# Kernel optimization log

Measured on AMD Instinct MI355X. Metric: run time of the kernel, lower is better.

Reference implementation:

```python
import jax, jax.numpy as jnp
import numpy as np

N_HEADS = 16
MAX_DIST = 64


def setup_inputs() -> dict:
    key = jax.random.key(0)
    ks = jax.random.split(key, 7)
    B, S, D = 16, 512, 1024
    hd = D // N_HEADS
    num_rel = 2 * MAX_DIST + 1
    s = 0.02
    return {
        "x": jax.random.normal(ks[0], (B, S, D), dtype=jnp.float32),
        "Wq": jax.random.normal(ks[1], (D, D), dtype=jnp.float32) * s,
        "Wk": jax.random.normal(ks[2], (D, D), dtype=jnp.float32) * s,
        "Wv": jax.random.normal(ks[3], (D, D), dtype=jnp.float32) * s,
        "Eq": jax.random.normal(ks[4], (num_rel, hd), dtype=jnp.float32) * s,
        "Ek": jax.random.normal(ks[5], (num_rel, hd), dtype=jnp.float32) * s,
        "Ev": jax.random.normal(ks[6], (num_rel, hd), dtype=jnp.float32) * s,
    }


def reference(x, Wq, Wk, Wv, Eq, Ek, Ev):
    B, S, D = x.shape
    H = N_HEADS
    hd = D // H
    # relative position index matrix, values in [0, 2*max_dist]
    r = jnp.arange(S)
    rel = jnp.clip(r[:, None] - r[None, :], -MAX_DIST, MAX_DIST) + MAX_DIST  # (S,S)

    def proj(W):
        return jnp.einsum('bsd,de->bse', x, W).reshape(B, S, H, hd).transpose(0, 2, 1, 3)

    q, k, v = proj(Wq), proj(Wk), proj(Wv)  # (B,H,S,hd)

    a_q = Eq[rel]  # (S,S,hd)
    a_k = Ek[rel]
    a_v = Ev[rel]

    content = jnp.einsum('bhld,bhmd->bhlm', q, k)
    rel_k = jnp.einsum('bhld,lmd->bhlm', q, a_k)
    rel_q = jnp.einsum('bhmd,lmd->bhlm', k, a_q)
    pos_pos = jnp.einsum('lmd,lmd->lm', a_q, a_k)

    scale = 1.0 / (hd ** 0.5)
    logits = (content + rel_k + rel_q + pos_pos) * scale
    attn = jax.nn.softmax(logits, axis=-1)

    out = jnp.einsum('bhlm,bhmd->bhld', attn, v) + jnp.einsum('bhlm,lmd->bhld', attn, a_v)
    return out.transpose(0, 2, 1, 3).reshape(B, S, D)
```

## Files before the change

kernel.cpp:

```cpp
#include <hip/hip_runtime.h>

#define SEQ 512
#define NH 16
#define HD 64
#define NREL 129
#define ER 136
#define SCALE 0.125f

typedef __attribute__((ext_vector_type(8))) short bf16x8;
typedef __attribute__((ext_vector_type(4))) float f32x4;

__device__ __forceinline__ unsigned short f2bf(float x) {
    unsigned u = __builtin_bit_cast(unsigned, x);
    u += 0x7FFFu + ((u >> 16) & 1u);
    return (unsigned short)(u >> 16);
}
__device__ __forceinline__ float bf2f(unsigned short s) {
    unsigned u = ((unsigned)s) << 16;
    return __builtin_bit_cast(float, u);
}
__device__ __forceinline__ unsigned pack2(float a, float b) {
    return (unsigned)f2bf(a) | ((unsigned)f2bf(b) << 16);
}
__device__ __forceinline__ void gld_lds16(const uint4* g, uint4* l) {
    __builtin_amdgcn_global_load_lds(
        (const __attribute__((address_space(1))) unsigned int*)(g),
        (__attribute__((address_space(3))) unsigned int*)(l),
        16, 0, 0);
}

__global__ __launch_bounds__(256) void conv_x(const float* __restrict__ in,
                                              unsigned short* __restrict__ ob) {
    size_t i = (size_t)blockIdx.x * 256 + threadIdx.x;
    const float4* p = (const float4*)in + i * 2;
    float4 a = p[0], b = p[1];
    uint4 o;
    o.x = pack2(a.x, a.y); o.y = pack2(a.z, a.w);
    o.z = pack2(b.x, b.y); o.w = pack2(b.z, b.w);
    ((uint4*)ob)[i] = o;
}

__global__ __launch_bounds__(256) void conv_w(const float* __restrict__ Wq,
                                              const float* __restrict__ Wk,
                                              const float* __restrict__ Wv,
                                              unsigned short* __restrict__ WbT) {
    __shared__ float Ws[64][65];
    const int t = threadIdx.x;
    const int mi = blockIdx.x >> 8;
    const int rem = blockIdx.x & 255;
    const int k0 = (rem >> 4) * 64, n0 = (rem & 15) * 64;
    const float* W = mi == 0 ? Wq : (mi == 1 ? Wk : Wv);
    const int rr = t >> 4, c4 = (t & 15) * 4;
#pragma unroll
    for (int j = 0; j < 4; j++) {
        float4 v = *(const float4*)&W[(size_t)(k0 + rr + j * 16) * 1024 + n0 + c4];
        Ws[rr + j * 16][c4 + 0] = v.x; Ws[rr + j * 16][c4 + 1] = v.y;
        Ws[rr + j * 16][c4 + 2] = v.z; Ws[rr + j * 16][c4 + 3] = v.w;
    }
    __syncthreads();
    const int n = t >> 2;
    for (int cc = (t & 3); cc < 8; cc += 4) {
        unsigned short tmp[8];
#pragma unroll
        for (int j = 0; j < 8; j++) tmp[j] = f2bf(Ws[cc * 8 + j][n]);
        *(uint4*)&WbT[(size_t)(mi * 1024 + n0 + n) * 1024 + k0 + cc * 8] = *(uint4*)tmp;
    }
}

__global__ void conv_e(const float* __restrict__ Eq, const float* __restrict__ Ek,
                       unsigned short* __restrict__ Eqb, unsigned short* __restrict__ Ekb) {
    const int t = threadIdx.x;
    for (int i = t; i < 1152; i += 256) {
        int r = i >> 3, c8 = (i & 7) * 8;
        uint4 oq = {0, 0, 0, 0}, ok = {0, 0, 0, 0};
        if (r < NREL) {
            float4 a = *(const float4*)&Eq[r * 64 + c8];
            float4 b = *(const float4*)&Eq[r * 64 + c8 + 4];
            oq.x = pack2(a.x, a.y); oq.y = pack2(a.z, a.w);
            oq.z = pack2(b.x, b.y); oq.w = pack2(b.z, b.w);
            float4 c = *(const float4*)&Ek[r * 64 + c8];
            float4 d = *(const float4*)&Ek[r * 64 + c8 + 4];
            ok.x = pack2(c.x, c.y); ok.y = pack2(c.z, c.w);
            ok.z = pack2(d.x, d.y); ok.w = pack2(d.z, d.w);
        }
        ((uint4*)Eqb)[i] = oq;
        ((uint4*)Ekb)[i] = ok;
    }
}

__global__ void ee_k(const float* __restrict__ Eq, const float* __restrict__ Ek,
                     float* __restrict__ ee) {
    int r = threadIdx.x;
    if (r < NREL) {
        float s = 0.f;
        for (int d = 0; d < HD; d++) s += Eq[r * HD + d] * Ek[r * HD + d];
        ee[r] = s;
    }
}

__global__ __launch_bounds__(256) void proj_mfma(const unsigned short* __restrict__ xb,
                                                 const unsigned short* __restrict__ WbT,
                                                 unsigned short* __restrict__ Qb,
                                                 unsigned short* __restrict__ Kb,
                                                 unsigned short* __restrict__ Vb) {
    __shared__ uint4 smem[2176];
    const int t = threadIdx.x;
    const int bm = blockIdx.x & 63;
    const int bn = blockIdx.x >> 6;
    const int m0 = bm * 128;
    const int n0g = bn * 128;
    const int w = t >> 6, lane = t & 63, ln = lane & 15, kg = lane >> 4;
    const int wm = w >> 1, wn = w & 1;
    const int lrow = lane >> 3;
    const int lcol = lane & 7;

    f32x4 acc[4][4];
#pragma unroll
    for (int i = 0; i < 4; i++)
#pragma unroll
        for (int j = 0; j < 4; j++) acc[i][j] = (f32x4){0.f, 0.f, 0.f, 0.f};

    const uint4* gA[4]; const uint4* gB[4]; uint4* lA[4]; uint4* lB[4];
#pragma unroll
    for (int j = 0; j < 4; j++) {
        const int seg = w * 4 + j;
        gA[j] = (const uint4*)xb  + (size_t)(m0  + seg * 8 + lrow) * 128 + lcol;
        gB[j] = (const uint4*)WbT + (size_t)(n0g + seg * 8 + lrow) * 128 + lcol;
        lA[j] = smem + seg * 64;
        lB[j] = smem + 1024 + seg * 64;
    }

    for (int kt = 0; kt < 16; ++kt) {
        __syncthreads();
#pragma unroll
        for (int j = 0; j < 4; j++) {
            gld_lds16(gA[j] + kt * 8, lA[j]);
            gld_lds16(gB[j] + kt * 8, lB[j]);
        }
        __syncthreads();
#pragma unroll
        for (int ks = 0; ks < 2; ks++) {
            bf16x8 af[4], bfr[4];
            const int ch = ks * 4 + kg;
#pragma unroll
            for (int i = 0; i < 4; i++) af[i]  = *(const bf16x8*)(smem + (wm * 64 + i * 16 + ln) * 8 + ch);
#pragma unroll
            for (int j = 0; j < 4; j++) bfr[j] = *(const bf16x8*)(smem + 1024 + (wn * 64 + j * 16 + ln) * 8 + ch);
#pragma unroll
            for (int i = 0; i < 4; i++)
#pragma unroll
                for (int j = 0; j < 4; j++)
                    acc[i][j] = __builtin_amdgcn_mfma_f32_16x16x32_bf16(af[i], bfr[j], acc[i][j], 0, 0, 0);
        }
    }
    __syncthreads();
    short (*cs)[136] = (short(*)[136])smem;
#pragma unroll
    for (int i = 0; i < 4; i++)
#pragma unroll
        for (int j = 0; j < 4; j++)
#pragma unroll
            for (int reg = 0; reg < 4; reg++)
                cs[wm * 64 + i * 16 + kg * 4 + reg][wn * 64 + j * 16 + ln] = (short)f2bf(acc[i][j][reg]);
    __syncthreads();
    const int which = n0g >> 10;
    unsigned short* outp = which == 0 ? Qb : (which == 1 ? Kb : Vb);
    const int ncol0 = n0g & 1023;
#pragma unroll
    for (int j = 0; j < 8; j++) {
        int id = j * 256 + t;
        int r = id >> 4, c = id & 15;
        *((uint4*)(outp + (size_t)(m0 + r) * 1024 + ncol0) + c) = *((const uint4*)&cs[r][0] + c);
    }
}

__global__ __launch_bounds__(256) void qk_e_mfma(const unsigned short* __restrict__ Qb,
                                                 const unsigned short* __restrict__ Kb,
                                                 const unsigned short* __restrict__ Ekb,
                                                 const unsigned short* __restrict__ Eqb,
                                                 const float* __restrict__ ee,
                                                 unsigned short* __restrict__ qEe,
                                                 unsigned short* __restrict__ kEb) {
    __shared__ uint4 lds[3328];
    __shared__ float eeS[136];
    uint4* Qt = lds;
    uint4* Kt = lds + 512;
    uint4* EkS = lds + 1024;
    uint4* EqS = lds + 2176;
    const int t = threadIdx.x, w = t >> 6, lane = t & 63, ln = lane & 15, kg = lane >> 4;
    const int g0 = blockIdx.x * 64;

    {
        int r = t >> 2, cb = (t & 3) * 2;
        const uint4* qg = (const uint4*)Qb + (size_t)(g0 + r) * 8;
        const uint4* kgp = (const uint4*)Kb + (size_t)(g0 + r) * 8;
#pragma unroll
        for (int j = 0; j < 2; j++) {
            int c = cb + j;
            Qt[r * 8 + (c ^ (r & 7))] = qg[c];
            Kt[r * 8 + (c ^ (r & 7))] = kgp[c];
        }
    }
    for (int i = t; i < 1152; i += 256) {
        int r = i >> 3, c = i & 7;
        EkS[r * 8 + (c ^ (r & 7))] = ((const uint4*)Ekb)[i];
        EqS[r * 8 + (c ^ (r & 7))] = ((const uint4*)Eqb)[i];
    }
    if (t < NREL) eeS[t] = ee[t];
    __syncthreads();

    const int lx = ln & 7;
    {
        bf16x8 a0 = *(bf16x8*)&Qt[(w * 16 + ln) * 8 + (kg ^ lx)];
        bf16x8 a1 = *(bf16x8*)&Qt[(w * 16 + ln) * 8 + ((4 + kg) ^ lx)];
        f32x4 acc[9];
#pragma unroll
        for (int j = 0; j < 9; j++) acc[j] = (f32x4){0.f, 0.f, 0.f, 0.f};
#pragma unroll
        for (int j = 0; j < 9; j++) {
            acc[j] = __builtin_amdgcn_mfma_f32_16x16x32_bf16(a0, *(bf16x8*)&EkS[(j * 16 + ln) * 8 + (kg ^ lx)], acc[j], 0, 0, 0);
            acc[j] = __builtin_amdgcn_mfma_f32_16x16x32_bf16(a1, *(bf16x8*)&EkS[(j * 16 + ln) * 8 + ((4 + kg) ^ lx)], acc[j], 0, 0, 0);
        }
#pragma unroll
        for (int j = 0; j < 9; j++) {
            int r = j * 16 + ln;
            if (r <= 128) {
#pragma unroll
                for (int reg = 0; reg < 4; reg++) {
                    int g = g0 + w * 16 + kg * 4 + reg;
                    qEe[(size_t)g * ER + r] = f2bf(acc[j][reg] + eeS[r]);
                }
            }
        }
    }
    {
        bf16x8 a0 = *(bf16x8*)&Kt[(w * 16 + ln) * 8 + (kg ^ lx)];
        bf16x8 a1 = *(bf16x8*)&Kt[(w * 16 + ln) * 8 + ((4 + kg) ^ lx)];
        f32x4 acc[9];
#pragma unroll
        for (int j = 0; j < 9; j++) acc[j] = (f32x4){0.f, 0.f, 0.f, 0.f};
#pragma unroll
        for (int j = 0; j < 9; j++) {
            acc[j] = __builtin_amdgcn_mfma_f32_16x16x32_bf16(a0, *(bf16x8*)&EqS[(j * 16 + ln) * 8 + (kg ^ lx)], acc[j], 0, 0, 0);
            acc[j] = __builtin_amdgcn_mfma_f32_16x16x32_bf16(a1, *(bf16x8*)&EqS[(j * 16 + ln) * 8 + ((4 + kg) ^ lx)], acc[j], 0, 0, 0);
        }
#pragma unroll
        for (int j = 0; j < 9; j++) {
            int r = j * 16 + ln;
            if (r <= 128) {
#pragma unroll
                for (int reg = 0; reg < 4; reg++) {
                    int g = g0 + w * 16 + kg * 4 + reg;
                    kEb[(size_t)g * ER + r] = f2bf(acc[j][reg]);
                }
            }
        }
    }
}

__global__ __launch_bounds__(256) void attn_k(const unsigned short* __restrict__ Q,
                                              const unsigned short* __restrict__ K,
                                              const unsigned short* __restrict__ V,
                                              const unsigned short* __restrict__ qEg,
                                              const unsigned short* __restrict__ kEg,
                                              const float* __restrict__ Ev,
                                              float* __restrict__ out) {
    __shared__ __align__(16) char un[18432];
    __shared__ short qEeS[64][ER];
    __shared__ short Pt[4][16][40];
    __shared__ short aRs[4][16][ER];
    __shared__ float invs[4][16];

    short (*Qsb)[64] = (short(*)[64])un;
    short (*Kt)[72]  = (short(*)[72])un;
    short* Vtt       = (short*)(un + 4608);
    short (*kEt)[ER] = (short(*)[ER])(un + 9728);
    short (*EvT)[ER] = (short(*)[ER])un;

    const int t = threadIdx.x;
    const int g = blockIdx.x;
    const int lt = (g >> 3) & 7;
    const int bh = ((g >> 6) << 3) | (g & 7);
    const int b = bh >> 4, h = bh & 15;
    const int bS = b * SEQ;
    const int l0 = lt * 64;
    const int w = t >> 6;
    const int lane = t & 63;
    const int ln = lane & 15;
    const int kg = lane >> 4;
    const int l0w = l0 + w * 16;

    for (int i = t; i < 512; i += 256) {
        int r = i >> 3, c8 = (i & 7) * 8;
        *(uint4*)&Qsb[r][c8] = *(const uint4*)&Q[(size_t)(bS + l0 + r) * 1024 + h * 64 + c8];
    }
    for (int i = t; i < 1088; i += 256) {
        int r = i / 17, c = i % 17;
        ((uint4*)&qEeS[r][0])[c] = ((const uint4*)&qEg[(size_t)((bS + l0 + r) * NH + h) * ER])[c];
    }
    for (int i = t; i < 4352; i += 256) ((unsigned*)aRs)[i] = 0u;
    __syncthreads();

    bf16x8 qf0 = *(bf16x8*)&Qsb[w * 16 + ln][kg * 8];
    bf16x8 qf1 = *(bf16x8*)&Qsb[w * 16 + ln][32 + kg * 8];

    const int sr = t >> 3;
    const int sc8 = (t & 7) * 8;
    const unsigned short* Kg0 = K + (size_t)(bS + sr) * 1024 + h * 64 + sc8;
    const unsigned short* Vg0 = V + (size_t)(bS + sr) * 1024 + h * 64 + sc8;
    const int r0 = t / 17,          c0 = t % 17;
    const int r1 = (t + 256) / 17,  c1 = (t + 256) % 17;
    const int r2 = (t + 512) / 17,  c2 = (t + 512) % 17;
    const unsigned short* kE0 = kEg + ((size_t)(bS + r0) * NH + h) * ER;
    const unsigned short* kE1 = kEg + ((size_t)(bS + r1) * NH + h) * ER;
    const unsigned short* kE2 = kEg + ((size_t)(bS + r2) * NH + h) * ER;

    uint4 kv, vv, ke0, ke1, ke2;
    kv  = *(const uint4*)(Kg0);
    vv  = *(const uint4*)(Vg0);
    ke0 = ((const uint4*)kE0)[c0];
    ke1 = ((const uint4*)kE1)[c1];
    if (t < 32) ke2 = ((const uint4*)kE2)[c2];

    f32x4 of[4];
#pragma unroll
    for (int nt = 0; nt < 4; nt++) of[nt] = (f32x4){0.f, 0.f, 0.f, 0.f};
    float rs[4]   = {0.f, 0.f, 0.f, 0.f};
    float s0[4]   = {0.f, 0.f, 0.f, 0.f};
    float s128[4] = {0.f, 0.f, 0.f, 0.f};

    const int vkey = (t & 7) & 3;
    for (int mt = 0; mt < 16; mt++) {
        const int m0 = mt * 32;
        __syncthreads();
        *(uint4*)&Kt[sr][sc8] = kv;
        {
            const short* vs = (const short*)&vv;
#pragma unroll
            for (int j = 0; j < 8; j++) {
                const int d = sc8 + j;
                Vtt[d * 40 + ((((sr >> 3) ^ vkey)) << 3) + (sr & 7)] = vs[j];
            }
        }
        ((uint4*)&kEt[r0][0])[c0] = ke0;
        ((uint4*)&kEt[r1][0])[c1] = ke1;
        if (t < 32) ((uint4*)&kEt[r2][0])[c2] = ke2;
        if (mt < 15) {
            const size_t koff = (size_t)(mt + 1) * 32 * 1024;
            const size_t eoff = (size_t)(mt + 1) * 32 * NH * ER;
            kv  = *(const uint4*)(Kg0 + koff);
            vv  = *(const uint4*)(Vg0 + koff);
            ke0 = ((const uint4*)(kE0 + eoff))[c0];
            ke1 = ((const uint4*)(kE1 + eoff))[c1];
            if (t < 32) ke2 = ((const uint4*)(kE2 + eoff))[c2];
        }
        __syncthreads();

#pragma unroll
        for (int sub = 0; sub < 2; sub++) {
            f32x4 acc = (f32x4){0.f, 0.f, 0.f, 0.f};
            acc = __builtin_amdgcn_mfma_f32_16x16x32_bf16(qf0, *(bf16x8*)&Kt[sub * 16 + ln][kg * 8], acc, 0, 0, 0);
            acc = __builtin_amdgcn_mfma_f32_16x16x32_bf16(qf1, *(bf16x8*)&Kt[sub * 16 + ln][32 + kg * 8], acc, 0, 0, 0);
            const int mloc = sub * 16 + ln;
            const int m = m0 + mloc;
#pragma unroll
            for (int reg = 0; reg < 4; reg++) {
                const int lr = kg * 4 + reg;
                const int dlt = (l0w + lr) - m;
                const int r = dlt < -64 ? 0 : (dlt > 64 ? 128 : dlt + 64);
                float lg = (acc[reg] + bf2f((unsigned short)qEeS[w * 16 + lr][r])
                                     + bf2f((unsigned short)kEt[mloc][r])) * SCALE;
                float p = __expf(lg);
                rs[reg] += p;
                if (dlt >= 64)       s128[reg] += p;
                else if (dlt <= -64) s0[reg]   += p;
                else                 aRs[w][lr][r] = (short)f2bf(p);
                Pt[w][lr][mloc] = (short)f2bf(p);
            }
        }
        asm volatile("" ::: "memory");
        bf16x8 pf = *(bf16x8*)&Pt[w][ln][kg * 8];
#pragma unroll
        for (int nt = 0; nt < 4; nt++) {
            const int d = nt * 16 + ln;
            const bf16x8 vf = *(const bf16x8*)&Vtt[d * 40 + ((kg ^ ((d >> 3) & 3)) << 3)];
            of[nt] = __builtin_amdgcn_mfma_f32_16x16x32_bf16(pf, vf, of[nt], 0, 0, 0);
        }
    }

    __syncthreads();
#pragma unroll
    for (int reg = 0; reg < 4; reg++) {
        for (int off = 1; off <= 8; off <<= 1) {
            rs[reg]   += __shfl_xor(rs[reg], off);
            s0[reg]   += __shfl_xor(s0[reg], off);
            s128[reg] += __shfl_xor(s128[reg], off);
        }
    }
    float inv[4];
#pragma unroll
    for (int reg = 0; reg < 4; reg++) inv[reg] = 1.0f / rs[reg];

    if (ln == 0) {
#pragma unroll
        for (int reg = 0; reg < 4; reg++) {
            aRs[w][kg * 4 + reg][0]   = (short)f2bf(s0[reg]   * inv[reg]);
            aRs[w][kg * 4 + reg][128] = (short)f2bf(s128[reg] * inv[reg]);
            invs[w][kg * 4 + reg] = inv[reg];
        }
    }
    for (int i = t; i < 8256; i += 256) {
        int r = i >> 6, d = i & 63;
        EvT[d][r] = (short)f2bf(Ev[i]);
    }
    __syncthreads();
    {
        const int row = lane >> 2;
        const float sc = invs[w][row];
#pragma unroll
        for (int kk = 0; kk < 32; kk++) {
            int c = (lane & 3) * 32 + kk;
            if (c >= 1) aRs[w][row][c] = (short)f2bf(bf2f((unsigned short)aRs[w][row][c]) * sc);
        }
    }
#pragma unroll
    for (int nt = 0; nt < 4; nt++)
#pragma unroll
        for (int reg = 0; reg < 4; reg++) of[nt][reg] *= inv[reg];
    __syncthreads();

    f32x4 o2[4];
#pragma unroll
    for (int nt = 0; nt < 4; nt++) o2[nt] = (f32x4){0.f, 0.f, 0.f, 0.f};
#pragma unroll
    for (int nt = 0; nt < 4; nt++)
#pragma unroll
        for (int ks = 0; ks < 4; ks++)
            o2[nt] = __builtin_amdgcn_mfma_f32_16x16x32_bf16(*(bf16x8*)&aRs[w][ln][ks * 32 + kg * 8],
                                                             *(bf16x8*)&EvT[nt * 16 + ln][ks * 32 + kg * 8],
                                                             o2[nt], 0, 0, 0);
#pragma unroll
    for (int nt = 0; nt < 4; nt++) {
        const float e128 = bf2f((unsigned short)EvT[nt * 16 + ln][128]);
#pragma unroll
        for (int reg = 0; reg < 4; reg++) {
            const int lr = kg * 4 + reg;
            const float a128 = bf2f((unsigned short)aRs[w][lr][128]);
            out[(size_t)(bS + l0w + lr) * 1024 + h * 64 + nt * 16 + ln] =
                of[nt][reg] + o2[nt][reg] + a128 * e128;
        }
    }
}

extern "C" void kernel_launch(void* const* d_in, const int* in_sizes, int n_in,
                              void* d_out, int out_size, void* d_ws, size_t ws_size,
                              hipStream_t stream) {
    const float* x  = (const float*)d_in[0];
    const float* Wq = (const float*)d_in[1];
    const float* Wk = (const float*)d_in[2];
    const float* Wv = (const float*)d_in[3];
    const float* Eq = (const float*)d_in[4];
    const float* Ek = (const float*)d_in[5];
    const float* Ev = (const float*)d_in[6];
    float* out = (float*)d_out;
    char* ws = (char*)d_ws;

    unsigned short* Qb  = (unsigned short*)(ws);
    unsigned short* Kb  = (unsigned short*)(ws + 16777216ull);
    unsigned short* Vb  = (unsigned short*)(ws + 33554432ull);
    unsigned short* xb  = (unsigned short*)(ws + 50331648ull);
    unsigned short* WbT = (unsigned short*)(ws + 67108864ull);
    unsigned short* Ekb = (unsigned short*)(ws + 73400320ull);
    unsigned short* Eqb = (unsigned short*)(ws + 73418752ull);
    float*          ee  = (float*)(ws + 73437184ull);
    unsigned short* qEe = (unsigned short*)(ws + 73437760ull);
    unsigned short* kEb = (unsigned short*)(ws + 109089344ull);

    conv_x<<<4096, 256, 0, stream>>>(x, xb);
    conv_w<<<768, 256, 0, stream>>>(Wq, Wk, Wv, WbT);
    conv_e<<<1, 256, 0, stream>>>(Eq, Ek, Eqb, Ekb);
    ee_k<<<1, 256, 0, stream>>>(Eq, Ek, ee);
    proj_mfma<<<1536, 256, 0, stream>>>(xb, WbT, Qb, Kb, Vb);
    qk_e_mfma<<<2048, 256, 0, stream>>>(Qb, Kb, Ekb, Eqb, ee, qEe, kEb);
    attn_k<<<2048, 256, 0, stream>>>(Qb, Kb, Vb, qEe, kEb, Ev, out);
}
```

Before: 262.0 us.

## Split attention work across 8 waves per block along key and output dims

The attention kernel now runs 512 threads per block instead of 256. Each group of four waves handles one half of every 32-key tile and one half of the output head dimension. K/V staging and relative-embedding staging are split between the two wave groups, and the row sums are reduced through shared memory. This doubles the waves available to hide latency and spreads the exp/softmax work, at the cost of an extra barrier per tile and cross-wave reductions.

```diff
diff --git a/kernel.cpp b/kernel.cpp
--- a/kernel.cpp
+++ b/kernel.cpp
@@ -258,7 +258,7 @@
     }
 }
 
-__global__ __launch_bounds__(256) void attn_k(const unsigned short* __restrict__ Q,
+__global__ __launch_bounds__(512) void attn_k(const unsigned short* __restrict__ Q,
                                               const unsigned short* __restrict__ K,
                                               const unsigned short* __restrict__ V,
                                               const unsigned short* __restrict__ qEg,
@@ -267,9 +267,12 @@
                                               float* __restrict__ out) {
     __shared__ __align__(16) char un[18432];
     __shared__ short qEeS[64][ER];
-    __shared__ short Pt[4][16][40];
+    __shared__ short Pt[8][16][20];
     __shared__ short aRs[4][16][ER];
-    __shared__ float invs[4][16];
+    __shared__ float rsB[2][64];
+    __shared__ float s0B[2][64];
+    __shared__ float s128B[2][64];
+    __shared__ float invs[64];
 
     short (*Qsb)[64] = (short(*)[64])un;
     short (*Kt)[72]  = (short(*)[72])un;
@@ -288,103 +291,119 @@
     const int lane = t & 63;
     const int ln = lane & 15;
     const int kg = lane >> 4;
-    const int l0w = l0 + w * 16;
-
-    for (int i = t; i < 512; i += 256) {
-        int r = i >> 3, c8 = (i & 7) * 8;
+    const int gq = w & 3;
+    const int msub = w >> 2;
+    const int ntb = msub * 2;
+    const int l0w = l0 + gq * 16;
+
+    {
+        int r = t >> 3, c8 = (t & 7) * 8;
         *(uint4*)&Qsb[r][c8] = *(const uint4*)&Q[(size_t)(bS + l0 + r) * 1024 + h * 64 + c8];
     }
-    for (int i = t; i < 1088; i += 256) {
+    for (int i = t; i < 1088; i += 512) {
         int r = i / 17, c = i % 17;
         ((uint4*)&qEeS[r][0])[c] = ((const uint4*)&qEg[(size_t)((bS + l0 + r) * NH + h) * ER])[c];
     }
-    for (int i = t; i < 4352; i += 256) ((unsigned*)aRs)[i] = 0u;
-    __syncthreads();
-
-    bf16x8 qf0 = *(bf16x8*)&Qsb[w * 16 + ln][kg * 8];
-    bf16x8 qf1 = *(bf16x8*)&Qsb[w * 16 + ln][32 + kg * 8];
-
-    const int sr = t >> 3;
+    for (int i = t; i < 4352; i += 512) ((unsigned*)aRs)[i] = 0u;
+    __syncthreads();
+
+    bf16x8 qf0 = *(bf16x8*)&Qsb[gq * 16 + ln][kg * 8];
+    bf16x8 qf1 = *(bf16x8*)&Qsb[gq * 16 + ln][32 + kg * 8];
+
+    const int sr = (t & 255) >> 3;
     const int sc8 = (t & 7) * 8;
     const unsigned short* Kg0 = K + (size_t)(bS + sr) * 1024 + h * 64 + sc8;
     const unsigned short* Vg0 = V + (size_t)(bS + sr) * 1024 + h * 64 + sc8;
-    const int r0 = t / 17,          c0 = t % 17;
-    const int r1 = (t + 256) / 17,  c1 = (t + 256) % 17;
-    const int r2 = (t + 512) / 17,  c2 = (t + 512) % 17;
+    const int u = t & 255;
+    const int r0 = u / 17,          c0 = u % 17;
+    const int r1 = (u + 256) / 17,  c1 = (u + 256) % 17;
+    const int r2 = (u + 512) / 17,  c2 = (u + 512) % 17;
     const unsigned short* kE0 = kEg + ((size_t)(bS + r0) * NH + h) * ER;
     const unsigned short* kE1 = kEg + ((size_t)(bS + r1) * NH + h) * ER;
     const unsigned short* kE2 = kEg + ((size_t)(bS + r2) * NH + h) * ER;
 
     uint4 kv, vv, ke0, ke1, ke2;
-    kv  = *(const uint4*)(Kg0);
-    vv  = *(const uint4*)(Vg0);
-    ke0 = ((const uint4*)kE0)[c0];
-    ke1 = ((const uint4*)kE1)[c1];
-    if (t < 32) ke2 = ((const uint4*)kE2)[c2];
-
-    f32x4 of[4];
-#pragma unroll
-    for (int nt = 0; nt < 4; nt++) of[nt] = (f32x4){0.f, 0.f, 0.f, 0.f};
+    if (w < 4) {
+        kv = *(const uint4*)(Kg0);
+        vv = *(const uint4*)(Vg0);
+    } else {
+        ke0 = ((const uint4*)kE0)[c0];
+        ke1 = ((const uint4*)kE1)[c1];
+        if (u < 32) ke2 = ((const uint4*)kE2)[c2];
+    }
+
+    f32x4 of[2];
+    of[0] = (f32x4){0.f, 0.f, 0.f, 0.f};
+    of[1] = (f32x4){0.f, 0.f, 0.f, 0.f};
     float rs[4]   = {0.f, 0.f, 0.f, 0.f};
     float s0[4]   = {0.f, 0.f, 0.f, 0.f};
     float s128[4] = {0.f, 0.f, 0.f, 0.f};
 
     const int vkey = (t & 7) & 3;
+    const int mloc = msub * 16 + ln;
+
     for (int mt = 0; mt < 16; mt++) {
         const int m0 = mt * 32;
         __syncthreads();
-        *(uint4*)&Kt[sr][sc8] = kv;
-        {
+        if (w < 4) {
+            *(uint4*)&Kt[sr][sc8] = kv;
             const short* vs = (const short*)&vv;
 #pragma unroll
             for (int j = 0; j < 8; j++) {
                 const int d = sc8 + j;
                 Vtt[d * 40 + ((((sr >> 3) ^ vkey)) << 3) + (sr & 7)] = vs[j];
             }
-        }
-        ((uint4*)&kEt[r0][0])[c0] = ke0;
-        ((uint4*)&kEt[r1][0])[c1] = ke1;
-        if (t < 32) ((uint4*)&kEt[r2][0])[c2] = ke2;
+        } else {
+            ((uint4*)&kEt[r0][0])[c0] = ke0;
+            ((uint4*)&kEt[r1][0])[c1] = ke1;
+            if (u < 32) ((uint4*)&kEt[r2][0])[c2] = ke2;
+        }
         if (mt < 15) {
             const size_t koff = (size_t)(mt + 1) * 32 * 1024;
             const size_t eoff = (size_t)(mt + 1) * 32 * NH * ER;
-            kv  = *(const uint4*)(Kg0 + koff);
-            vv  = *(const uint4*)(Vg0 + koff);
-            ke0 = ((const uint4*)(kE0 + eoff))[c0];
-            ke1 = ((const uint4*)(kE1 + eoff))[c1];
-            if (t < 32) ke2 = ((const uint4*)(kE2 + eoff))[c2];
+            if (w < 4) {
+                kv = *(const uint4*)(Kg0 + koff);
+                vv = *(const uint4*)(Vg0 + koff);
+            } else {
+                ke0 = ((const uint4*)(kE0 + eoff))[c0];
+                ke1 = ((const uint4*)(kE1 + eoff))[c1];
+                if (u < 32) ke2 = ((const uint4*)(kE2 + eoff))[c2];
+            }
         }
         __syncthreads();
 
-#pragma unroll
-        for (int sub = 0; sub < 2; sub++) {
-            f32x4 acc = (f32x4){0.f, 0.f, 0.f, 0.f};
-            acc = __builtin_amdgcn_mfma_f32_16x16x32_bf16(qf0, *(bf16x8*)&Kt[sub * 16 + ln][kg * 8], acc, 0, 0, 0);
-            acc = __builtin_amdgcn_mfma_f32_16x16x32_bf16(qf1, *(bf16x8*)&Kt[sub * 16 + ln][32 + kg * 8], acc, 0, 0, 0);
-            const int mloc = sub * 16 + ln;
-            const int m = m0 + mloc;
-#pragma unroll
-            for (int reg = 0; reg < 4; reg++) {
-                const int lr = kg * 4 + reg;
-                const int dlt = (l0w + lr) - m;
-                const int r = dlt < -64 ? 0 : (dlt > 64 ? 128 : dlt + 64);
-                float lg = (acc[reg] + bf2f((unsigned short)qEeS[w * 16 + lr][r])
-                                     + bf2f((unsigned short)kEt[mloc][r])) * SCALE;
-                float p = __expf(lg);
-                rs[reg] += p;
-                if (dlt >= 64)       s128[reg] += p;
-                else if (dlt <= -64) s0[reg]   += p;
-                else                 aRs[w][lr][r] = (short)f2bf(p);
-                Pt[w][lr][mloc] = (short)f2bf(p);
-            }
-        }
-        asm volatile("" ::: "memory");
-        bf16x8 pf = *(bf16x8*)&Pt[w][ln][kg * 8];
-#pragma unroll
-        for (int nt = 0; nt < 4; nt++) {
-            const int d = nt * 16 + ln;
+        const int m = m0 + mloc;
+        int rr[4]; float qe[4], kev[4];
+#pragma unroll
+        for (int reg = 0; reg < 4; reg++) {
+            const int lr = gq * 16 + kg * 4 + reg;
+            const int dlt = (l0 + lr) - m;
+            rr[reg] = min(max(dlt, -64), 64) + 64;
+            qe[reg]  = bf2f((unsigned short)qEeS[lr][rr[reg]]);
+            kev[reg] = bf2f((unsigned short)kEt[mloc][rr[reg]]);
+        }
+        f32x4 acc = (f32x4){0.f, 0.f, 0.f, 0.f};
+        acc = __builtin_amdgcn_mfma_f32_16x16x32_bf16(qf0, *(bf16x8*)&Kt[mloc][kg * 8], acc, 0, 0, 0);
+        acc = __builtin_amdgcn_mfma_f32_16x16x32_bf16(qf1, *(bf16x8*)&Kt[mloc][32 + kg * 8], acc, 0, 0, 0);
+#pragma unroll
+        for (int reg = 0; reg < 4; reg++) {
+            const int lr = kg * 4 + reg;
+            const int dlt = (l0w + lr) - m;
+            float p = __expf((acc[reg] + qe[reg] + kev[reg]) * SCALE);
+            rs[reg] += p;
+            if (dlt >= 64)       s128[reg] += p;
+            else if (dlt <= -64) s0[reg]   += p;
+            else                 aRs[gq][lr][rr[reg]] = (short)f2bf(p);
+            Pt[w][lr][ln] = (short)f2bf(p);
+        }
+        __syncthreads();
+
+        bf16x8 pf = *(bf16x8*)&Pt[gq + ((kg >> 1) << 2)][ln][(kg & 1) * 8];
+#pragma unroll
+        for (int i = 0; i < 2; i++) {
+            const int d = (ntb + i) * 16 + ln;
             const bf16x8 vf = *(const bf16x8*)&Vtt[d * 40 + ((kg ^ ((d >> 3) & 3)) << 3)];
-            of[nt] = __builtin_amdgcn_mfma_f32_16x16x32_bf16(pf, vf, of[nt], 0, 0, 0);
+            of[i] = __builtin_amdgcn_mfma_f32_16x16x32_bf16(pf, vf, of[i], 0, 0, 0);
         }
     }
 
@@ -397,57 +416,74 @@
             s128[reg] += __shfl_xor(s128[reg], off);
         }
     }
-    float inv[4];
-#pragma unroll
-    for (int reg = 0; reg < 4; reg++) inv[reg] = 1.0f / rs[reg];
-
     if (ln == 0) {
 #pragma unroll
         for (int reg = 0; reg < 4; reg++) {
-            aRs[w][kg * 4 + reg][0]   = (short)f2bf(s0[reg]   * inv[reg]);
-            aRs[w][kg * 4 + reg][128] = (short)f2bf(s128[reg] * inv[reg]);
-            invs[w][kg * 4 + reg] = inv[reg];
-        }
-    }
-    for (int i = t; i < 8256; i += 256) {
-        int r = i >> 6, d = i & 63;
-        EvT[d][r] = (short)f2bf(Ev[i]);
-    }
-    __syncthreads();
-    {
+            const int row = gq * 16 + kg * 4 + reg;
+            rsB[msub][row]   = rs[reg];
+            s0B[msub][row]   = s0[reg];
+            s128B[msub][row] = s128[reg];
+        }
+    }
+    __syncthreads();
+    float inv[4], a128[4];
+#pragma unroll
+    for (int reg = 0; reg < 4; reg++) {
+        const int row = gq * 16 + kg * 4 + reg;
+        const float rt = rsB[0][row] + rsB[1][row];
+        inv[reg] = 1.0f / rt;
+        a128[reg] = (s128B[0][row] + s128B[1][row]) * inv[reg];
+    }
+    if (w < 4) {
+        if (ln == 0) {
+#pragma unroll
+            for (int reg = 0; reg < 4; reg++) {
+                const int row = gq * 16 + kg * 4 + reg;
+                aRs[gq][kg * 4 + reg][0] = (short)f2bf((s0B[0][row] + s0B[1][row]) * inv[reg]);
+                invs[row] = inv[reg];
+            }
+        }
+    } else {
+        for (int i = t - 256; i < 8256; i += 256) {
+            int r = i >> 6, d = i & 63;
+            EvT[d][r] = (short)f2bf(Ev[i]);
+        }
+    }
+    __syncthreads();
+    if (w < 4) {
         const int row = lane >> 2;
-        const float sc = invs[w][row];
+        const float sc = invs[gq * 16 + row];
 #pragma unroll
         for (int kk = 0; kk < 32; kk++) {
             int c = (lane & 3) * 32 + kk;
-            if (c >= 1) aRs[w][row][c] = (short)f2bf(bf2f((unsigned short)aRs[w][row][c]) * sc);
-        }
-    }
-#pragma unroll
-    for (int nt = 0; nt < 4; nt++)
-#pragma unroll
-        for (int reg = 0; reg < 4; reg++) of[nt][reg] *= inv[reg];
-    __syncthreads();
-
-    f32x4 o2[4];
-#pragma unroll
-    for (int nt = 0; nt < 4; nt++) o2[nt] = (f32x4){0.f, 0.f, 0.f, 0.f};
-#pragma unroll
-    for (int nt = 0; nt < 4; nt++)
+            if (c >= 1) aRs[gq][row][c] = (short)f2bf(bf2f((unsigned short)aRs[gq][row][c]) * sc);
+        }
+    }
+#pragma unroll
+    for (int i = 0; i < 2; i++)
+#pragma unroll
+        for (int reg = 0; reg < 4; reg++) of[i][reg] *= inv[reg];
+    __syncthreads();
+
+    f32x4 o2[2];
+    o2[0] = (f32x4){0.f, 0.f, 0.f, 0.f};
+    o2[1] = (f32x4){0.f, 0.f, 0.f, 0.f};
+#pragma unroll
+    for (int i = 0; i < 2; i++)
 #pragma unroll
         for (int ks = 0; ks < 4; ks++)
-            o2[nt] = __builtin_amdgcn_mfma_f32_16x16x32_bf16(*(bf16x8*)&aRs[w][ln][ks * 32 + kg * 8],
-                                                             *(bf16x8*)&EvT[nt * 16 + ln][ks * 32 + kg * 8],
-                                                             o2[nt], 0, 0, 0);
-#pragma unroll
-    for (int nt = 0; nt < 4; nt++) {
+            o2[i] = __builtin_amdgcn_mfma_f32_16x16x32_bf16(*(bf16x8*)&aRs[gq][ln][ks * 32 + kg * 8],
+                                                            *(bf16x8*)&EvT[(ntb + i) * 16 + ln][ks * 32 + kg * 8],
+                                                            o2[i], 0, 0, 0);
+#pragma unroll
+    for (int i = 0; i < 2; i++) {
+        const int nt = ntb + i;
         const float e128 = bf2f((unsigned short)EvT[nt * 16 + ln][128]);
 #pragma unroll
         for (int reg = 0; reg < 4; reg++) {
             const int lr = kg * 4 + reg;
-            const float a128 = bf2f((unsigned short)aRs[w][lr][128]);
             out[(size_t)(bS + l0w + lr) * 1024 + h * 64 + nt * 16 + ln] =
-                of[nt][reg] + o2[nt][reg] + a128 * e128;
+                of[i][reg] + o2[i][reg] + a128[reg] * e128;
         }
     }
 }
@@ -482,5 +518,5 @@
     ee_k<<<1, 256, 0, stream>>>(Eq, Ek, ee);
     proj_mfma<<<1536, 256, 0, stream>>>(xb, WbT, Qb, Kb, Vb);
     qk_e_mfma<<<2048, 256, 0, stream>>>(Qb, Kb, Ekb, Eqb, ee, qEe, kEb);
-    attn_k<<<2048, 256, 0, stream>>>(Qb, Kb, Vb, qEe, kEb, Ev, out);
-}
+    attn_k<<<2048, 512, 0, stream>>>(Qb, Kb, Vb, qEe, kEb, Ev, out);
+}
```

Result: faster. 248.0 us (-5.3%).
